# Kernel tuning notes

Hardware: AMD Instinct MI355X
Metric: run time of the kernel (lower is better)

## Reference

```python
import jax, jax.numpy as jnp
import numpy as np

B, S, D, H = 2, 2048, 1024, 16
DH = D // H


def setup_inputs() -> dict:
    key = jax.random.key(0)
    ks = jax.random.split(key, 6)
    scale = 1.0 / np.sqrt(D)
    x = jax.random.normal(ks[0], (B, S, D), dtype=jnp.float32)
    mask = jnp.tril(jnp.ones((S, S), dtype=jnp.int32))  # causal 0/1 mask
    Wq = jax.random.normal(ks[1], (D, D), dtype=jnp.float32) * scale
    Wk = jax.random.normal(ks[2], (D, D), dtype=jnp.float32) * scale
    Wv = jax.random.normal(ks[3], (D, D), dtype=jnp.float32) * scale
    Wo = jax.random.normal(ks[4], (D, D), dtype=jnp.float32) * scale
    z = jnp.zeros((D,), dtype=jnp.float32)
    return {"x": x, "mask": mask, "Wq": Wq, "bq": z, "Wk": Wk, "bk": z,
            "Wv": Wv, "bv": z, "Wo": Wo, "bo": z}


def reference(x, mask, Wq, bq, Wk, bk, Wv, bv, Wo, bo):
    # Linear projections (torch Linear: x @ W.T + b; here W stored as [in, out])
    Q = x @ Wq + bq
    K = x @ Wk + bk
    V = x @ Wv + bv
    # [B, S, D] -> [B, H, S, DH]
    Q = Q.reshape(B, S, H, DH).transpose(0, 2, 1, 3)
    K = K.reshape(B, S, H, DH).transpose(0, 2, 1, 3)
    V = V.reshape(B, S, H, DH).transpose(0, 2, 1, 3)
    # scores: [B, H, S, S]
    attn = jnp.einsum('bhqd,bhkd->bhqk', Q, K) / jnp.sqrt(jnp.float32(DH))
    attn = jnp.where(mask == 0, jnp.float32(-1e9), attn)
    scores = jax.nn.softmax(attn, axis=-1)
    # dropout is identity in eval mode
    out = jnp.einsum('bhqk,bhkd->bhqd', scores, V)
    out = out.transpose(0, 2, 1, 3).reshape(B, S, D)
    return out @ Wo + bo
```

## Files before the change

kernel.cpp:

```cpp
#include <hip/hip_runtime.h>
#include <hip/hip_bf16.h>


typedef short bf16x8 __attribute__((ext_vector_type(8)));
typedef float f32x4  __attribute__((ext_vector_type(4)));
typedef short s16x4  __attribute__((ext_vector_type(4)));

#define BB 2
#define SS 2048
#define DD 1024
#define HH 16
#define DHH 64

__device__ __forceinline__ unsigned short f2bf(float f) {
    unsigned u = __builtin_bit_cast(unsigned, f);
    u += 0x7FFFu + ((u >> 16) & 1u);
    return (unsigned short)(u >> 16);
}
__device__ __forceinline__ unsigned short f2bf_trunc(float f) {
    return (unsigned short)(__builtin_bit_cast(unsigned, f) >> 16);
}
__device__ __forceinline__ void cp16(const unsigned short* g, unsigned short* l) {
    __builtin_amdgcn_global_load_lds(
        (const __attribute__((address_space(1))) unsigned int*)(g),
        (__attribute__((address_space(3))) unsigned int*)(l), 16, 0, 0);
}

__global__ __launch_bounds__(256) void prep(
    const float* __restrict__ x,
    const float* __restrict__ w0, const float* __restrict__ w1,
    const float* __restrict__ w2, const float* __restrict__ w3,
    unsigned short* __restrict__ xbf, unsigned short* __restrict__ wt) {
    __shared__ float tile[64][65];
    const int bid = blockIdx.x;
    const int tid = threadIdx.x;
    if (bid < 4096) {
        int i = (bid * 256 + tid) * 4;
        float4 v = *reinterpret_cast<const float4*>(x + i);
        s16x4 p;
        p[0] = (short)f2bf(v.x); p[1] = (short)f2bf(v.y);
        p[2] = (short)f2bf(v.z); p[3] = (short)f2bf(v.w);
        *reinterpret_cast<s16x4*>(xbf + i) = p;
        return;
    }
    const int tb = bid - 4096;
    const int z  = tb >> 8;
    const int bx = (tb & 15) * 64, by = ((tb >> 4) & 15) * 64;
    const float* src = z == 0 ? w0 : z == 1 ? w1 : z == 2 ? w2 : w3;
    unsigned short* out = wt + (size_t)z * (DD * DD);
    const int tx = tid & 63, ty = tid >> 6;
    #pragma unroll
    for (int i = 0; i < 64; i += 4)
        tile[ty + i][tx] = src[(size_t)(by + ty + i) * DD + bx + tx];
    __syncthreads();
    #pragma unroll
    for (int i = 0; i < 64; i += 4)
        out[(size_t)(bx + ty + i) * DD + by + tx] = f2bf(tile[tx][ty + i]);
}

__global__ __launch_bounds__(256) void gemm_qkv(
    const unsigned short* __restrict__ A, const unsigned short* __restrict__ Wt,
    const float* __restrict__ b0, const float* __restrict__ b1,
    const float* __restrict__ b2,
    unsigned short* __restrict__ d0, unsigned short* __restrict__ d1,
    unsigned short* __restrict__ d2) {
    __shared__ __align__(16) unsigned short As[128 * 64];
    __shared__ __align__(16) unsigned short Bs[128 * 64];

    const int tid  = threadIdx.x;
    const int lane = tid & 63;
    const int w    = tid >> 6;
    const int col  = lane & 15;
    const int quad = lane >> 4;
    const int wm   = (w >> 1) * 64;
    const int wn   = (w & 1) * 64;
    const int mb   = blockIdx.y * 128;
    const int nb   = blockIdx.x * 128;

    const int r8 = lane >> 3, gg = lane & 7;
    const int srcoff = ((gg ^ r8) * 8);
    const int cswz = col & 7;

    f32x4 acc[4][4];
    #pragma unroll
    for (int i = 0; i < 4; i++)
        #pragma unroll
        for (int j = 0; j < 4; j++) acc[i][j] = (f32x4){0.f, 0.f, 0.f, 0.f};

    for (int kt = 0; kt < 1024; kt += 64) {
        __syncthreads();
        #pragma unroll
        for (int it = 0; it < 4; it++) {
            int row = w * 32 + it * 8 + r8;
            cp16(A  + (size_t)(mb + row) * 1024 + kt + srcoff, As + (w * 32 + it * 8) * 64);
            cp16(Wt + (size_t)(nb + row) * 1024 + kt + srcoff, Bs + (w * 32 + it * 8) * 64);
        }
        __syncthreads();
        #pragma unroll
        for (int kk = 0; kk < 64; kk += 32) {
            const int kg = (kk >> 3) + quad;
            const int pos = ((kg ^ cswz) * 8);
            bf16x8 af[4], bfr[4];
            #pragma unroll
            for (int i = 0; i < 4; i++)
                af[i] = *reinterpret_cast<const bf16x8*>(As + (wm + i * 16 + col) * 64 + pos);
            #pragma unroll
            for (int j = 0; j < 4; j++)
                bfr[j] = *reinterpret_cast<const bf16x8*>(Bs + (wn + j * 16 + col) * 64 + pos);
            #pragma unroll
            for (int i = 0; i < 4; i++)
                #pragma unroll
                for (int j = 0; j < 4; j++)
                    acc[i][j] = __builtin_amdgcn_mfma_f32_16x16x32_bf16(af[i], bfr[j], acc[i][j], 0, 0, 0);
        }
    }

    const float QSCALE = 0.125f * 1.44269504f;
    #pragma unroll
    for (int i = 0; i < 4; i++) {
        int mg = mb + wm + i * 16 + quad * 4;
        #pragma unroll
        for (int j = 0; j < 4; j++) {
            int ng = nb + wn + j * 16 + col;
            int sel = ng >> 10, n2 = ng & 1023;
            int h = n2 >> 6, dd2 = n2 & 63;
            int b = mg >> 11, s = mg & 2047;
            int bh = b * HH + h;
            const float* bp = sel == 0 ? b0 : sel == 1 ? b1 : b2;
            float bbv = bp[n2];
            if (sel == 0) {
                #pragma unroll
                for (int r = 0; r < 4; r++)
                    d0[((size_t)bh * SS + s + r) * DHH + dd2] = f2bf((acc[i][j][r] + bbv) * QSCALE);
            } else if (sel == 1) {
                #pragma unroll
                for (int r = 0; r < 4; r++)
                    d1[((size_t)bh * SS + s + r) * DHH + dd2] = f2bf(acc[i][j][r] + bbv);
            } else {
                s16x4 pack;
                #pragma unroll
                for (int r = 0; r < 4; r++) pack[r] = (short)f2bf(acc[i][j][r] + bbv);
                *reinterpret_cast<s16x4*>(d2 + ((size_t)bh * DHH + dd2) * SS + s) = pack;
            }
        }
    }
}

__global__ __launch_bounds__(256) void gemm_out(
    const unsigned short* __restrict__ A, const unsigned short* __restrict__ Wt,
    const float* __restrict__ b0, float* __restrict__ d0f) {
    __shared__ __align__(16) unsigned short As[128 * 64];
    __shared__ __align__(16) unsigned short Bs[64 * 64];

    const int tid  = threadIdx.x;
    const int lane = tid & 63;
    const int w    = tid >> 6;
    const int col  = lane & 15;
    const int quad = lane >> 4;
    const int wm   = (w >> 1) * 64;
    const int wn   = (w & 1) * 32;
    const int mb   = blockIdx.y * 128;
    const int nb   = blockIdx.x * 64;

    const int r8 = lane >> 3, gg = lane & 7;
    const int srcoff = ((gg ^ r8) * 8);
    const int cswz = col & 7;

    f32x4 acc[4][2];
    #pragma unroll
    for (int i = 0; i < 4; i++)
        #pragma unroll
        for (int j = 0; j < 2; j++) acc[i][j] = (f32x4){0.f, 0.f, 0.f, 0.f};

    for (int kt = 0; kt < 1024; kt += 64) {
        __syncthreads();
        #pragma unroll
        for (int it = 0; it < 4; it++) {
            int row = w * 32 + it * 8 + r8;
            cp16(A + (size_t)(mb + row) * 1024 + kt + srcoff, As + (w * 32 + it * 8) * 64);
        }
        cp16(Wt + (size_t)(nb + w * 16 + r8) * 1024 + kt + srcoff, Bs + (w * 16) * 64);
        cp16(Wt + (size_t)(nb + w * 16 + 8 + r8) * 1024 + kt + srcoff, Bs + (w * 16 + 8) * 64);
        __syncthreads();
        #pragma unroll
        for (int kk = 0; kk < 64; kk += 32) {
            const int kg = (kk >> 3) + quad;
            const int pos = ((kg ^ cswz) * 8);
            bf16x8 af[4], bfr[2];
            #pragma unroll
            for (int i = 0; i < 4; i++)
                af[i] = *reinterpret_cast<const bf16x8*>(As + (wm + i * 16 + col) * 64 + pos);
            #pragma unroll
            for (int j = 0; j < 2; j++)
                bfr[j] = *reinterpret_cast<const bf16x8*>(Bs + (wn + j * 16 + col) * 64 + pos);
            #pragma unroll
            for (int i = 0; i < 4; i++)
                #pragma unroll
                for (int j = 0; j < 2; j++)
                    acc[i][j] = __builtin_amdgcn_mfma_f32_16x16x32_bf16(af[i], bfr[j], acc[i][j], 0, 0, 0);
        }
    }

    #pragma unroll
    for (int i = 0; i < 4; i++) {
        int mg = mb + wm + i * 16 + quad * 4;
        #pragma unroll
        for (int j = 0; j < 2; j++) {
            int ng = nb + wn + j * 16 + col;
            float bbv = b0[ng];
            #pragma unroll
            for (int r = 0; r < 4; r++)
                d0f[(size_t)(mg + r) * 1024 + ng] = acc[i][j][r] + bbv;
        }
    }
}

__global__ __launch_bounds__(256, 4) void attn(
    const unsigned short* __restrict__ Q, const unsigned short* __restrict__ K,
    const unsigned short* __restrict__ Vt, unsigned short* __restrict__ O) {
    __shared__ __align__(16) unsigned short Ks[2][64 * 64];
    __shared__ __align__(16) unsigned short Vs[2][64 * 64];

    const int tid  = threadIdx.x;
    const int lane = tid & 63;
    const int w    = tid >> 6;
    const int col  = lane & 15;
    const int quad = lane >> 4;
    const int bh   = blockIdx.x & 31;
    const int qt   = 31 - (blockIdx.x >> 5);
    const int qb   = qt * 64;
    const int r8 = lane >> 3, gg = lane & 7;
    const int srcoff = ((gg ^ r8) * 8);
    const int cswz = col & 7;
    const int pos0 = (quad       ^ cswz) * 8;
    const int pos1 = ((4 + quad) ^ cswz) * 8;

    bf16x8 onesf;
    #pragma unroll
    for (int j = 0; j < 8; j++) onesf[j] = (col == 0) ? (short)0x3F80 : (short)0;

    const int qrow = qb + w * 16 + col;
    const size_t qbase = ((size_t)bh * SS + qrow) * DHH;
    bf16x8 qlo = *reinterpret_cast<const bf16x8*>(Q + qbase + quad * 8);
    bf16x8 qhi = *reinterpret_cast<const bf16x8*>(Q + qbase + 32 + quad * 8);

    f32x4 o[5];
    #pragma unroll
    for (int d = 0; d < 5; d++) o[d] = (f32x4){0.f, 0.f, 0.f, 0.f};
    float m_i = -1e30f;

    const int ntiles = qt + 1;
    for (int t0 = 0; t0 < ntiles; t0 += 2) {
        const bool two = (t0 + 1 < ntiles);
        __syncthreads();
        #pragma unroll
        for (int it = 0; it < 2; it++) {
            int drow = w * 16 + it * 8;
            int skey = (w >> 1) * 32 + it * 16 + (r8 >> 2) * 8 + (w & 1) * 4 + (r8 & 3);
            cp16(K  + ((size_t)bh * SS + t0 * 64 + skey) * DHH + srcoff,
                 Ks[0] + drow * 64);
            cp16(Vt + ((size_t)bh * DHH + drow + r8) * SS + t0 * 64 + srcoff,
                 Vs[0] + drow * 64);
        }
        if (two) {
            #pragma unroll
            for (int it = 0; it < 2; it++) {
                int drow = w * 16 + it * 8;
                int skey = (w >> 1) * 32 + it * 16 + (r8 >> 2) * 8 + (w & 1) * 4 + (r8 & 3);
                cp16(K  + ((size_t)bh * SS + (t0 + 1) * 64 + skey) * DHH + srcoff,
                     Ks[1] + drow * 64);
                cp16(Vt + ((size_t)bh * DHH + drow + r8) * SS + (t0 + 1) * 64 + srcoff,
                     Vs[1] + drow * 64);
            }
        }
        __syncthreads();

        f32x4 sc[8];
        #pragma unroll
        for (int nt = 0; nt < 4; nt++) {
            int krow = nt * 16 + col;
            bf16x8 klo = *reinterpret_cast<const bf16x8*>(Ks[0] + krow * 64 + pos0);
            bf16x8 khi = *reinterpret_cast<const bf16x8*>(Ks[0] + krow * 64 + pos1);
            f32x4 z = (f32x4){0.f, 0.f, 0.f, 0.f};
            z = __builtin_amdgcn_mfma_f32_16x16x32_bf16(klo, qlo, z, 0, 0, 0);
            z = __builtin_amdgcn_mfma_f32_16x16x32_bf16(khi, qhi, z, 0, 0, 0);
            sc[nt] = z;
        }
        if (two) {
            #pragma unroll
            for (int nt = 0; nt < 4; nt++) {
                int krow = nt * 16 + col;
                bf16x8 klo = *reinterpret_cast<const bf16x8*>(Ks[1] + krow * 64 + pos0);
                bf16x8 khi = *reinterpret_cast<const bf16x8*>(Ks[1] + krow * 64 + pos1);
                f32x4 z = (f32x4){0.f, 0.f, 0.f, 0.f};
                z = __builtin_amdgcn_mfma_f32_16x16x32_bf16(klo, qlo, z, 0, 0, 0);
                z = __builtin_amdgcn_mfma_f32_16x16x32_bf16(khi, qhi, z, 0, 0, 0);
                sc[4 + nt] = z;
            }
        }
        if (t0 == qt || (two && t0 + 1 == qt)) {
            const int sb = (t0 == qt) ? 0 : 4;
            const int tb = (t0 == qt) ? t0 : t0 + 1;
            #pragma unroll
            for (int nt = 0; nt < 4; nt++) {
                #pragma unroll
                for (int r = 0; r < 4; r++) {
                    int kg = tb * 64 + (nt >> 1) * 32 + quad * 8 + (nt & 1) * 4 + r;
                    if (kg > qrow) sc[sb + nt][r] = -3.0e38f;
                }
            }
        }
        float mx = fmaxf(fmaxf(sc[0][0], sc[0][1]), fmaxf(sc[0][2], sc[0][3]));
        #pragma unroll
        for (int nt = 1; nt < 4; nt++)
            mx = fmaxf(mx, fmaxf(fmaxf(sc[nt][0], sc[nt][1]), fmaxf(sc[nt][2], sc[nt][3])));
        if (two) {
            #pragma unroll
            for (int nt = 4; nt < 8; nt++)
                mx = fmaxf(mx, fmaxf(fmaxf(sc[nt][0], sc[nt][1]), fmaxf(sc[nt][2], sc[nt][3])));
        }
        mx = fmaxf(mx, __shfl_xor(mx, 16));
        mx = fmaxf(mx, __shfl_xor(mx, 32));
        float mnew = fmaxf(m_i, mx);
        bool upd = (mnew > m_i);
        if (__any(upd)) {
            float delta = m_i - mnew;
            #pragma unroll
            for (int r = 0; r < 4; r++) {
                float a = exp2f(__shfl(delta, quad * 4 + r));
                #pragma unroll
                for (int d = 0; d < 5; d++) o[d][r] *= a;
            }
        }
        m_i = mnew;

        {
            bf16x8 pf0, pf1;
            #pragma unroll
            for (int j = 0; j < 8; j++) {
                pf0[j] = (short)f2bf_trunc(exp2f(sc[(j >> 2)][j & 3] - mnew));
                pf1[j] = (short)f2bf_trunc(exp2f(sc[2 + (j >> 2)][j & 3] - mnew));
            }
            #pragma unroll
            for (int dt = 0; dt < 4; dt++) {
                int rv = dt * 16 + col;
                bf16x8 vf0 = *reinterpret_cast<const bf16x8*>(Vs[0] + rv * 64 + pos0);
                bf16x8 vf1 = *reinterpret_cast<const bf16x8*>(Vs[0] + rv * 64 + pos1);
                o[dt] = __builtin_amdgcn_mfma_f32_16x16x32_bf16(pf0, vf0, o[dt], 0, 0, 0);
                o[dt] = __builtin_amdgcn_mfma_f32_16x16x32_bf16(pf1, vf1, o[dt], 0, 0, 0);
            }
            o[4] = __builtin_amdgcn_mfma_f32_16x16x32_bf16(pf0, onesf, o[4], 0, 0, 0);
            o[4] = __builtin_amdgcn_mfma_f32_16x16x32_bf16(pf1, onesf, o[4], 0, 0, 0);
        }
        if (two) {
            bf16x8 pf0, pf1;
            #pragma unroll
            for (int j = 0; j < 8; j++) {
                pf0[j] = (short)f2bf_trunc(exp2f(sc[4 + (j >> 2)][j & 3] - mnew));
                pf1[j] = (short)f2bf_trunc(exp2f(sc[6 + (j >> 2)][j & 3] - mnew));
            }
            #pragma unroll
            for (int dt = 0; dt < 4; dt++) {
                int rv = dt * 16 + col;
                bf16x8 vf0 = *reinterpret_cast<const bf16x8*>(Vs[1] + rv * 64 + pos0);
                bf16x8 vf1 = *reinterpret_cast<const bf16x8*>(Vs[1] + rv * 64 + pos1);
                o[dt] = __builtin_amdgcn_mfma_f32_16x16x32_bf16(pf0, vf0, o[dt], 0, 0, 0);
                o[dt] = __builtin_amdgcn_mfma_f32_16x16x32_bf16(pf1, vf1, o[dt], 0, 0, 0);
            }
            o[4] = __builtin_amdgcn_mfma_f32_16x16x32_bf16(pf0, onesf, o[4], 0, 0, 0);
            o[4] = __builtin_amdgcn_mfma_f32_16x16x32_bf16(pf1, onesf, o[4], 0, 0, 0);
        }
    }

    #pragma unroll
    for (int r = 0; r < 4; r++) {
        float lv = __shfl(o[4][r], lane & 48);
        float inv = 1.0f / lv;
        int sq = qb + w * 16 + quad * 4 + r;
        size_t base = ((size_t)(bh >> 4) * SS + sq) * DD + (size_t)(bh & 15) * DHH;
        #pragma unroll
        for (int dt = 0; dt < 4; dt++)
            O[base + dt * 16 + col] = f2bf(o[dt][r] * inv);
    }
}

extern "C" void kernel_launch(void* const* d_in, const int* in_sizes, int n_in,
                              void* d_out, int out_size, void* d_ws, size_t ws_size,
                              hipStream_t stream) {
    (void)in_sizes; (void)n_in; (void)out_size; (void)ws_size;
    const float* x  = (const float*)d_in[0];
    const float* Wq = (const float*)d_in[2];
    const float* bq = (const float*)d_in[3];
    const float* Wk = (const float*)d_in[4];
    const float* bk = (const float*)d_in[5];
    const float* Wv = (const float*)d_in[6];
    const float* bv = (const float*)d_in[7];
    const float* Wo = (const float*)d_in[8];
    const float* bo = (const float*)d_in[9];
    float* out = (float*)d_out;

    char* ws = (char*)d_ws;
    unsigned short* xbf = (unsigned short*)(ws);
    unsigned short* qws = (unsigned short*)(ws + ((size_t)8  << 20));
    unsigned short* kws = (unsigned short*)(ws + ((size_t)16 << 20));
    unsigned short* vws = (unsigned short*)(ws + ((size_t)24 << 20));
    unsigned short* wt  = (unsigned short*)(ws + ((size_t)32 << 20));
    unsigned short* ows = xbf;

    prep<<<dim3(5120), 256, 0, stream>>>(x, Wq, Wk, Wv, Wo, xbf, wt);
    gemm_qkv<<<dim3(24, 32), 256, 0, stream>>>(xbf, wt, bq, bk, bv,
                                               qws, kws, vws);
    attn<<<dim3(1024), 256, 0, stream>>>(qws, kws, vws, ows);
    gemm_out<<<dim3(16, 32), 256, 0, stream>>>(ows, wt + (size_t)3 * 1024 * 1024,
                                               bo, out);
}
```

Measured before the change: 200.7 us.

## Double-buffer QKV GEMM with 256x256 tiles and prefetch of next K-stage

The QKV projection GEMM moves from 128x128 tiles with 4 waves to 256x256 tiles with 8 waves, and double-buffers its LDS. The next K-slice is loaded asynchronously while MFMAs run on the current one, with per-phase barriers and s_setprio to interleave loads and math. The aim is to hide global-to-LDS latency and raise arithmetic intensity per block. The trade-offs are about 128KB of LDS per block and a grid of only 192 blocks, which is fewer than the CU count and leaves some CUs idle.

```diff
diff --git a/kernel.cpp b/kernel.cpp
--- a/kernel.cpp
+++ b/kernel.cpp
@@ -58,70 +58,97 @@
         out[(size_t)(bx + ty + i) * DD + by + tx] = f2bf(tile[tx][ty + i]);
 }
 
-__global__ __launch_bounds__(256) void gemm_qkv(
+__global__ __launch_bounds__(512, 2) void gemm_qkv(
     const unsigned short* __restrict__ A, const unsigned short* __restrict__ Wt,
     const float* __restrict__ b0, const float* __restrict__ b1,
     const float* __restrict__ b2,
     unsigned short* __restrict__ d0, unsigned short* __restrict__ d1,
     unsigned short* __restrict__ d2) {
-    __shared__ __align__(16) unsigned short As[128 * 64];
-    __shared__ __align__(16) unsigned short Bs[128 * 64];
+    __shared__ __align__(16) unsigned short As_[2][256 * 64];
+    __shared__ __align__(16) unsigned short Bs_[2][256 * 64];
 
     const int tid  = threadIdx.x;
     const int lane = tid & 63;
     const int w    = tid >> 6;
     const int col  = lane & 15;
     const int quad = lane >> 4;
-    const int wm   = (w >> 1) * 64;
-    const int wn   = (w & 1) * 64;
-    const int mb   = blockIdx.y * 128;
-    const int nb   = blockIdx.x * 128;
+    const int wr   = w >> 2;
+    const int wc   = w & 3;
+    const int mb   = blockIdx.y * 256;
+    const int nb   = blockIdx.x * 256;
 
     const int r8 = lane >> 3, gg = lane & 7;
     const int srcoff = ((gg ^ r8) * 8);
     const int cswz = col & 7;
-
-    f32x4 acc[4][4];
-    #pragma unroll
-    for (int i = 0; i < 4; i++)
+    const int pos0 = (quad       ^ cswz) * 8;
+    const int pos1 = ((4 + quad) ^ cswz) * 8;
+
+    f32x4 acc[8][4];
+    #pragma unroll
+    for (int i = 0; i < 8; i++)
         #pragma unroll
         for (int j = 0; j < 4; j++) acc[i][j] = (f32x4){0.f, 0.f, 0.f, 0.f};
 
+    auto stage = [&](int b, int kt) {
+        #pragma unroll
+        for (int i = 0; i < 4; i++) {
+            int rb = i * 64 + w * 8;
+            cp16(A  + (size_t)(mb + rb + r8) * 1024 + kt + srcoff,
+                 As_[b] + rb * 64);
+            cp16(Wt + (size_t)(nb + rb + r8) * 1024 + kt + srcoff,
+                 Bs_[b] + rb * 64);
+        }
+    };
+
+    int cur = 0;
+    stage(0, 0);
+    __syncthreads();
+
     for (int kt = 0; kt < 1024; kt += 64) {
+        if (kt + 64 < 1024) stage(cur ^ 1, kt + 64);
+        const unsigned short* Ab = As_[cur];
+        const unsigned short* Bb = Bs_[cur];
+        #pragma unroll
+        for (int p = 0; p < 4; p++) {
+            const int mh = p >> 1, nh = p & 1;
+            bf16x8 af0[4], af1[4], bq0[2], bq1[2];
+            #pragma unroll
+            for (int i = 0; i < 4; i++) {
+                const unsigned short* ap = Ab + (wr * 128 + mh * 64 + i * 16 + col) * 64;
+                af0[i] = *reinterpret_cast<const bf16x8*>(ap + pos0);
+                af1[i] = *reinterpret_cast<const bf16x8*>(ap + pos1);
+            }
+            #pragma unroll
+            for (int j = 0; j < 2; j++) {
+                const unsigned short* bp = Bb + (wc * 64 + nh * 32 + j * 16 + col) * 64;
+                bq0[j] = *reinterpret_cast<const bf16x8*>(bp + pos0);
+                bq1[j] = *reinterpret_cast<const bf16x8*>(bp + pos1);
+            }
+            __builtin_amdgcn_s_barrier();
+            __builtin_amdgcn_s_setprio(1);
+            #pragma unroll
+            for (int i = 0; i < 4; i++)
+                #pragma unroll
+                for (int j = 0; j < 2; j++) {
+                    acc[mh * 4 + i][nh * 2 + j] = __builtin_amdgcn_mfma_f32_16x16x32_bf16(
+                        af0[i], bq0[j], acc[mh * 4 + i][nh * 2 + j], 0, 0, 0);
+                    acc[mh * 4 + i][nh * 2 + j] = __builtin_amdgcn_mfma_f32_16x16x32_bf16(
+                        af1[i], bq1[j], acc[mh * 4 + i][nh * 2 + j], 0, 0, 0);
+                }
+            __builtin_amdgcn_s_setprio(0);
+            if (p < 3) __builtin_amdgcn_s_barrier();
+        }
         __syncthreads();
-        #pragma unroll
-        for (int it = 0; it < 4; it++) {
-            int row = w * 32 + it * 8 + r8;
-            cp16(A  + (size_t)(mb + row) * 1024 + kt + srcoff, As + (w * 32 + it * 8) * 64);
-            cp16(Wt + (size_t)(nb + row) * 1024 + kt + srcoff, Bs + (w * 32 + it * 8) * 64);
-        }
-        __syncthreads();
-        #pragma unroll
-        for (int kk = 0; kk < 64; kk += 32) {
-            const int kg = (kk >> 3) + quad;
-            const int pos = ((kg ^ cswz) * 8);
-            bf16x8 af[4], bfr[4];
-            #pragma unroll
-            for (int i = 0; i < 4; i++)
-                af[i] = *reinterpret_cast<const bf16x8*>(As + (wm + i * 16 + col) * 64 + pos);
-            #pragma unroll
-            for (int j = 0; j < 4; j++)
-                bfr[j] = *reinterpret_cast<const bf16x8*>(Bs + (wn + j * 16 + col) * 64 + pos);
-            #pragma unroll
-            for (int i = 0; i < 4; i++)
-                #pragma unroll
-                for (int j = 0; j < 4; j++)
-                    acc[i][j] = __builtin_amdgcn_mfma_f32_16x16x32_bf16(af[i], bfr[j], acc[i][j], 0, 0, 0);
-        }
+        cur ^= 1;
     }
 
     const float QSCALE = 0.125f * 1.44269504f;
     #pragma unroll
-    for (int i = 0; i < 4; i++) {
-        int mg = mb + wm + i * 16 + quad * 4;
-        #pragma unroll
-        for (int j = 0; j < 4; j++) {
-            int ng = nb + wn + j * 16 + col;
+    for (int mi = 0; mi < 8; mi++) {
+        int mg = mb + wr * 128 + mi * 16 + quad * 4;
+        #pragma unroll
+        for (int nj = 0; nj < 4; nj++) {
+            int ng = nb + wc * 64 + nj * 16 + col;
             int sel = ng >> 10, n2 = ng & 1023;
             int h = n2 >> 6, dd2 = n2 & 63;
             int b = mg >> 11, s = mg & 2047;
@@ -131,15 +158,15 @@
             if (sel == 0) {
                 #pragma unroll
                 for (int r = 0; r < 4; r++)
-                    d0[((size_t)bh * SS + s + r) * DHH + dd2] = f2bf((acc[i][j][r] + bbv) * QSCALE);
+                    d0[((size_t)bh * SS + s + r) * DHH + dd2] = f2bf((acc[mi][nj][r] + bbv) * QSCALE);
             } else if (sel == 1) {
                 #pragma unroll
                 for (int r = 0; r < 4; r++)
-                    d1[((size_t)bh * SS + s + r) * DHH + dd2] = f2bf(acc[i][j][r] + bbv);
+                    d1[((size_t)bh * SS + s + r) * DHH + dd2] = f2bf(acc[mi][nj][r] + bbv);
             } else {
                 s16x4 pack;
                 #pragma unroll
-                for (int r = 0; r < 4; r++) pack[r] = (short)f2bf(acc[i][j][r] + bbv);
+                for (int r = 0; r < 4; r++) pack[r] = (short)f2bf(acc[mi][nj][r] + bbv);
                 *reinterpret_cast<s16x4*>(d2 + ((size_t)bh * DHH + dd2) * SS + s) = pack;
             }
         }
@@ -408,7 +435,7 @@
     unsigned short* ows = xbf;
 
     prep<<<dim3(5120), 256, 0, stream>>>(x, Wq, Wk, Wv, Wo, xbf, wt);
-    gemm_qkv<<<dim3(24, 32), 256, 0, stream>>>(xbf, wt, bq, bk, bv,
+    gemm_qkv<<<dim3(12, 16), 512, 0, stream>>>(xbf, wt, bq, bk, bv,
                                                qws, kws, vws);
     attn<<<dim3(1024), 256, 0, stream>>>(qws, kws, vws, ows);
     gemm_out<<<dim3(16, 32), 256, 0, stream>>>(ows, wt + (size_t)3 * 1024 * 1024,
```

New measurement: 208.8 us. 4.0% more time.
